# Kernel tuning notes

Hardware: AMD Instinct MI355X
Metric: run time of the kernel (lower is better)

The kernel has to match this reference:

```python
import jax, jax.numpy as jnp
import numpy as np

EPS = 1e-5  # BatchNorm eps (torch default)


def gcn_conv(x, W, b, src, dst, ew, n_nodes):
    """PyG GCNConv with normalize=True, add_self_loops=True (fill_value=1.0).
    Self-loop contribution handled analytically instead of appending edges."""
    xw = x @ W  # [N, out]
    # degree including self-loop weight 1.0 (PyG sums weights at the target node)
    deg = jax.ops.segment_sum(ew, dst, num_segments=n_nodes) + 1.0  # [N]
    dinv = jnp.where(deg > 0, jax.lax.rsqrt(deg), 0.0)
    norm = dinv[src] * ew * dinv[dst]  # [E]
    agg = jax.ops.segment_sum(xw[src] * norm[:, None], dst, num_segments=n_nodes)
    agg = agg + xw * (dinv * dinv)[:, None]  # self-loop message
    return agg + b


def batch_norm(x, gamma, beta):
    m = jnp.mean(x, axis=0)
    v = jnp.var(x, axis=0)  # biased, matches torch BN normalization
    return gamma * (x - m) * jax.lax.rsqrt(v + EPS) + beta


def setup_inputs() -> dict:
    key = jax.random.key(0)
    ks = jax.random.split(key, 12)
    N, E, D_IN, D_H, D_OUT = 100000, 1600000, 128, 128, 40
    x = jax.random.normal(ks[0], (N, D_IN), dtype=jnp.float32)
    edge_index = jax.random.randint(ks[1], (2, E), 0, N, dtype=jnp.int64)
    edge_weight = jax.random.uniform(ks[2], (E,), dtype=jnp.float32)
    def lin(k, fi, fo):
        s = 1.0 / np.sqrt(fi)
        return jax.random.uniform(k, (fi, fo), dtype=jnp.float32, minval=-s, maxval=s)
    return {
        "x": x, "edge_index": edge_index, "edge_weight": edge_weight,
        "W0": lin(ks[3], D_IN, D_H), "b0": jnp.zeros((D_H,), jnp.float32),
        "g0": jnp.ones((D_H,), jnp.float32), "be0": jnp.zeros((D_H,), jnp.float32),
        "W1": lin(ks[4], D_H, D_H), "b1": jnp.zeros((D_H,), jnp.float32),
        "g1": jnp.ones((D_H,), jnp.float32), "be1": jnp.zeros((D_H,), jnp.float32),
        "W2": lin(ks[5], D_H, D_OUT), "b2": jnp.zeros((D_OUT,), jnp.float32),
    }


def reference(x, edge_index, edge_weight, W0, b0, g0, be0, W1, b1, g1, be1, W2, b2):
    n_nodes = x.shape[0]
    src, dst = edge_index[0], edge_index[1]
    # layer 0: GCNConv -> BN -> ReLU (dropout identity: deterministic/eval)
    h = gcn_conv(x, W0, b0, src, dst, edge_weight, n_nodes)
    h = jax.nn.relu(batch_norm(h, g0, be0))
    # layer 1
    h = gcn_conv(h, W1, b1, src, dst, edge_weight, n_nodes)
    h = jax.nn.relu(batch_norm(h, g1, be1))
    # last conv + log_softmax over classes
    h = gcn_conv(h, W2, b2, src, dst, edge_weight, n_nodes)
    return jax.nn.log_softmax(h, axis=-1)
```

## Files before the change

### kernel.cpp

```cpp
#include <hip/hip_runtime.h>
#include <math.h>


#define CHUNK 8192

typedef __attribute__((ext_vector_type(8))) short short8v;
typedef __attribute__((ext_vector_type(16))) float float16v;

__device__ __forceinline__ float2 bf2_unpack(unsigned u) {
    float2 r;
    r.x = __uint_as_float(u << 16);
    r.y = __uint_as_float(u & 0xffff0000u);
    return r;
}
__device__ __forceinline__ unsigned bf2_pack(float a, float b) {
    unsigned ua = __float_as_uint(a);
    unsigned ub = __float_as_uint(b);
    ua = (ua + 0x7fffu + ((ua >> 16) & 1u)) >> 16;
    ub = (ub + 0x7fffu + ((ub >> 16) & 1u)) >> 16;
    return ua | (ub << 16);
}
__device__ __forceinline__ short bf16r(float x) {
    unsigned u = __float_as_uint(x);
    u = (u + 0x7fffu + ((u >> 16) & 1u)) >> 16;
    return (short)u;
}
__device__ __forceinline__ short8v lds_read8(const short* p) {
    short4 lo = *(const short4*)p;
    short4 hi = *(const short4*)(p + 4);
    short8v r;
    r[0] = lo.x; r[1] = lo.y; r[2] = lo.z; r[3] = lo.w;
    r[4] = hi.x; r[5] = hi.y; r[6] = hi.z; r[7] = hi.w;
    return r;
}

__global__ void k_detect(const unsigned* __restrict__ raw, int nsample, int* __restrict__ flag) {
    int i = blockIdx.x * blockDim.x + threadIdx.x;
    if (i < nsample) {
        if (raw[2 * i + 1] != 0u) atomicOr(flag, 1);
    }
}

__device__ __forceinline__ int edge_src(const unsigned* raw, int e, int E, int is64) {
    return is64 ? (int)raw[2 * (size_t)e] : (int)raw[e];
}
__device__ __forceinline__ int edge_dst(const unsigned* raw, int e, int E, int is64) {
    return is64 ? (int)raw[2 * ((size_t)E + e)] : (int)raw[(size_t)E + e];
}

__global__ __launch_bounds__(256) void k_bhist(const unsigned* __restrict__ raw,
                                               int* __restrict__ bhist, int* __restrict__ chist,
                                               const int* __restrict__ flag,
                                               int E, int NB, int nchunks) {
    __shared__ int h[512];
    int is64 = (*flag == 0);
    for (int c = blockIdx.x; c < nchunks; c += gridDim.x) {
        for (int t = threadIdx.x; t < 512; t += 256) h[t] = 0;
        __syncthreads();
        int base = c * CHUNK;
        int end = (base + CHUNK < E) ? base + CHUNK : E;
        for (int e = base + threadIdx.x; e < end; e += 256) {
            int d = edge_dst(raw, e, E, is64);
            atomicAdd(&h[d >> 8], 1);
        }
        __syncthreads();
        for (int t = threadIdx.x; t < NB; t += 256) {
            int v = h[t];
            chist[(size_t)c * 512 + t] = v;
            if (v) atomicAdd(&bhist[t], v);
        }
        __syncthreads();
    }
}

__global__ __launch_bounds__(512) void k_bscan(const int* __restrict__ bhist,
                                               int* __restrict__ bstart,
                                               int* __restrict__ bcur, int NB) {
    __shared__ int s[512];
    int tid = threadIdx.x;
    int v = (tid < NB) ? bhist[tid] : 0;
    s[tid] = v;
    __syncthreads();
    for (int off = 1; off < 512; off <<= 1) {
        int t = (tid >= off) ? s[tid - off] : 0;
        __syncthreads();
        if (tid >= off) s[tid] += t;
        __syncthreads();
    }
    int ex = s[tid] - v;
    if (tid <= NB) {
        int val = (tid < NB) ? ex : s[NB > 0 ? NB - 1 : 0];
        bstart[tid] = val;
        if (tid < NB) bcur[tid] = val;
    }
}

__global__ __launch_bounds__(256) void k_part(const unsigned* __restrict__ raw,
                                              const float* __restrict__ ew,
                                              const int* __restrict__ chist,
                                              int* __restrict__ bcur, int2* __restrict__ staging,
                                              const int* __restrict__ flag,
                                              int E, int NB, int nchunks) {
    __shared__ int cur[512];
    int is64 = (*flag == 0);
    for (int c = blockIdx.x; c < nchunks; c += gridDim.x) {
        for (int t = threadIdx.x; t < NB; t += 256) {
            int v = chist[(size_t)c * 512 + t];
            cur[t] = v ? atomicAdd(&bcur[t], v) : 0;
        }
        __syncthreads();
        int base = c * CHUNK;
        int end = (base + CHUNK < E) ? base + CHUNK : E;
        for (int e = base + threadIdx.x; e < end; e += 256) {
            int s = edge_src(raw, e, E, is64);
            int d = edge_dst(raw, e, E, is64);
            float w = ew[e];
            int pos = atomicAdd(&cur[d >> 8], 1);
            staging[pos] = make_int2(s | ((d & 255) << 24), __float_as_int(w));
        }
        __syncthreads();
    }
}

__global__ __launch_bounds__(256) void k_bucket(const int* __restrict__ bstart,
                                                const int2* __restrict__ staging,
                                                int* __restrict__ rowptr, float* __restrict__ dinv,
                                                int2* __restrict__ ep, int N, int NB) {
    __shared__ int cnt[256];
    __shared__ float dw[256];
    __shared__ int sc[256];
    __shared__ int cur[256];

    const int b = blockIdx.x;
    const int t = threadIdx.x;
    const int n0 = b << 8;
    const int nn = (N - n0 < 256) ? (N - n0) : 256;
    const int es = bstart[b], ee = bstart[b + 1];

    cnt[t] = 0;
    dw[t] = 0.f;
    __syncthreads();

    for (int j = es + t; j < ee; j += 256) {
        int2 p = staging[j];
        int dl = ((unsigned)p.x) >> 24;
        atomicAdd(&cnt[dl], 1);
        atomicAdd(&dw[dl], __int_as_float(p.y));
    }
    __syncthreads();

    int v = cnt[t];
    sc[t] = v;
    __syncthreads();
    for (int off = 1; off < 256; off <<= 1) {
        int tv = (t >= off) ? sc[t - off] : 0;
        __syncthreads();
        if (t >= off) sc[t] += tv;
        __syncthreads();
    }
    int exoff = sc[t] - v;
    cur[t] = es + exoff;
    if (t < nn) {
        rowptr[n0 + t] = es + exoff;
        dinv[n0 + t] = rsqrtf(dw[t] + 1.0f);
    }
    if (t == 0) rowptr[(n0 + 256 < N) ? (n0 + 256) : N] = ee;
    __syncthreads();

    for (int j = es + t; j < ee; j += 256) {
        int2 p = staging[j];
        int dl = ((unsigned)p.x) >> 24;
        int pos = atomicAdd(&cur[dl], 1);
        ep[pos] = make_int2(p.x & 0x00ffffff, p.y);
    }
}

template <int DOUT, int NCT, bool BN, bool FP32IN>
__global__ __launch_bounds__(256) void k_gemm_mfma(
    const float* __restrict__ Xf, const unsigned* __restrict__ Xp,
    const float* __restrict__ W, const float* __restrict__ scale,
    const float* __restrict__ shift, const float* __restrict__ dscale,
    unsigned* __restrict__ Y, int N)
{
    constexpr int NDW = DOUT / 2;
    constexpr int LDK = 132;
    constexpr int WROWS = (NCT == 4) ? 128 : 64;
    constexpr int RTPW = (NCT == 4) ? 2 : 1;
    __shared__ short Wt[WROWS][LDK];
    __shared__ short As[64][LDK];
    __shared__ float scL[128], shL[128], dscL[64];

    const int tid = threadIdx.x;
    const int wv = tid >> 6, ln = tid & 63;
    const int m = ln & 31, q = ln >> 5;
    const int ct = wv % NCT;
    const int rtbase = (NCT == 4) ? 0 : (wv >> 1);

    if (BN && tid < 128) { scL[tid] = scale[tid]; shL[tid] = shift[tid]; }
    for (int i = tid; i < WROWS * 128; i += 256) {
        int n = i % WROWS, k = i / WROWS;
        float w = (n < DOUT) ? W[k * DOUT + n] : 0.f;
        Wt[n][k] = bf16r(w);
    }

    for (int base = blockIdx.x * 64; base < N; base += gridDim.x * 64) {
        __syncthreads();
        if (FP32IN) {
            for (int i = tid; i < 64 * 32; i += 256) {
                int r = i >> 5, s = i & 31;
                int row = base + r;
                float4 v = make_float4(0.f, 0.f, 0.f, 0.f);
                if (row < N) v = ((const float4*)(Xf + (size_t)row * 128))[s];
                short4 qv = make_short4(bf16r(v.x), bf16r(v.y), bf16r(v.z), bf16r(v.w));
                *(short4*)&As[r][s * 4] = qv;
            }
        } else {
            for (int i = tid; i < 64 * 16; i += 256) {
                int r = i >> 4, s = i & 15;
                int row = base + r;
                uint4 u = make_uint4(0, 0, 0, 0);
                if (row < N) u = ((const uint4*)(Xp + (size_t)row * 64))[s];
                unsigned uu[4] = {u.x, u.y, u.z, u.w};
                short vv[8];
#pragma unroll
                for (int d = 0; d < 4; d++) {
                    float2 f = bf2_unpack(uu[d]);
                    int fi = s * 8 + 2 * d;
                    f.x = fmaxf(f.x * scL[fi] + shL[fi], 0.f);
                    f.y = fmaxf(f.y * scL[fi + 1] + shL[fi + 1], 0.f);
                    vv[2 * d] = bf16r(f.x);
                    vv[2 * d + 1] = bf16r(f.y);
                }
                *(short4*)&As[r][s * 8] = make_short4(vv[0], vv[1], vv[2], vv[3]);
                *(short4*)&As[r][s * 8 + 4] = make_short4(vv[4], vv[5], vv[6], vv[7]);
            }
        }
        if (tid < 64) {
            int row = base + tid;
            dscL[tid] = (row < N) ? dscale[row] : 0.f;
        }
        __syncthreads();

        float16v acc[RTPW];
#pragma unroll
        for (int rt = 0; rt < RTPW; rt++)
#pragma unroll
            for (int r = 0; r < 16; r++) acc[rt][r] = 0.f;

#pragma unroll
        for (int kc = 0; kc < 8; kc++) {
            int kb = kc * 16 + q * 8;
            short8v bfrag = lds_read8(&Wt[ct * 32 + m][kb]);
#pragma unroll
            for (int rt = 0; rt < RTPW; rt++) {
                int rtg = (NCT == 4) ? rt : rtbase;
                short8v afrag = lds_read8(&As[rtg * 32 + m][kb]);
                acc[rt] = __builtin_amdgcn_mfma_f32_32x32x16_bf16(afrag, bfrag, acc[rt], 0, 0, 0);
            }
        }

#pragma unroll
        for (int rt = 0; rt < RTPW; rt++) {
            int rtg = (NCT == 4) ? rt : rtbase;
#pragma unroll
            for (int r = 0; r < 16; r++) {
                int rowl = rtg * 32 + (r & 3) + 8 * (r >> 2) + 4 * q;
                float v = acc[rt][r] * dscL[rowl];
                float pv = __shfl_xor(v, 1);
                if (!(ln & 1)) {
                    int row = base + rowl;
                    int cp = ct * 16 + (m >> 1);
                    if (row < N && cp < NDW)
                        __builtin_nontemporal_store(bf2_pack(v, pv), &Y[(size_t)row * NDW + cp]);
                }
            }
        }
    }
}

__global__ __launch_bounds__(256) void k_agg128(
    const unsigned* __restrict__ xw, const int* __restrict__ rowptr,
    const unsigned long long* __restrict__ ep, const float* __restrict__ dinv,
    const float* __restrict__ bias, unsigned* __restrict__ h,
    float* __restrict__ bn_sum, float* __restrict__ bn_sq, int N)
{
    __shared__ float redS[512], redQ[512];
    const int lane = threadIdx.x & 63;
    const int wave = threadIdx.x >> 6;
    const int base = blockIdx.x * 32 + wave * 8;
    const float b0 = bias[2 * lane], b1 = bias[2 * lane + 1];
    float s0 = 0.f, s1 = 0.f, q0 = 0.f, q1 = 0.f;

    const int nmax = (N - base < 8) ? (N - base) : 8;
    for (int n = 0; n < nmax; n++) {
        const int i = base + n;
        const int rs = rowptr[i], re = rowptr[i + 1];
        const float di = dinv[i];
        float2 sv = bf2_unpack(xw[(size_t)i * 64 + lane]);
        float acc0 = sv.x, acc1 = sv.y;
        int j = rs;
        for (; j + 8 <= re; j += 8) {
            unsigned long long u0 = __builtin_nontemporal_load(ep + j);
            unsigned long long u1 = __builtin_nontemporal_load(ep + j + 1);
            unsigned long long u2 = __builtin_nontemporal_load(ep + j + 2);
            unsigned long long u3 = __builtin_nontemporal_load(ep + j + 3);
            unsigned long long u4 = __builtin_nontemporal_load(ep + j + 4);
            unsigned long long u5 = __builtin_nontemporal_load(ep + j + 5);
            unsigned long long u6 = __builtin_nontemporal_load(ep + j + 6);
            unsigned long long u7 = __builtin_nontemporal_load(ep + j + 7);
            unsigned v0 = xw[(size_t)(unsigned)u0 * 64 + lane];
            unsigned v1 = xw[(size_t)(unsigned)u1 * 64 + lane];
            unsigned v2 = xw[(size_t)(unsigned)u2 * 64 + lane];
            unsigned v3 = xw[(size_t)(unsigned)u3 * 64 + lane];
            unsigned v4 = xw[(size_t)(unsigned)u4 * 64 + lane];
            unsigned v5 = xw[(size_t)(unsigned)u5 * 64 + lane];
            unsigned v6 = xw[(size_t)(unsigned)u6 * 64 + lane];
            unsigned v7 = xw[(size_t)(unsigned)u7 * 64 + lane];
            float c0 = __int_as_float((int)(u0 >> 32)), c1 = __int_as_float((int)(u1 >> 32));
            float c2 = __int_as_float((int)(u2 >> 32)), c3 = __int_as_float((int)(u3 >> 32));
            float c4 = __int_as_float((int)(u4 >> 32)), c5 = __int_as_float((int)(u5 >> 32));
            float c6 = __int_as_float((int)(u6 >> 32)), c7 = __int_as_float((int)(u7 >> 32));
            float2 f0 = bf2_unpack(v0), f1 = bf2_unpack(v1);
            float2 f2 = bf2_unpack(v2), f3 = bf2_unpack(v3);
            float2 f4 = bf2_unpack(v4), f5 = bf2_unpack(v5);
            float2 f6 = bf2_unpack(v6), f7 = bf2_unpack(v7);
            acc0 += c0 * f0.x + c1 * f1.x + c2 * f2.x + c3 * f3.x
                  + c4 * f4.x + c5 * f5.x + c6 * f6.x + c7 * f7.x;
            acc1 += c0 * f0.y + c1 * f1.y + c2 * f2.y + c3 * f3.y
                  + c4 * f4.y + c5 * f5.y + c6 * f6.y + c7 * f7.y;
        }
        for (; j + 4 <= re; j += 4) {
            unsigned long long u0 = __builtin_nontemporal_load(ep + j);
            unsigned long long u1 = __builtin_nontemporal_load(ep + j + 1);
            unsigned long long u2 = __builtin_nontemporal_load(ep + j + 2);
            unsigned long long u3 = __builtin_nontemporal_load(ep + j + 3);
            unsigned v0 = xw[(size_t)(unsigned)u0 * 64 + lane];
            unsigned v1 = xw[(size_t)(unsigned)u1 * 64 + lane];
            unsigned v2 = xw[(size_t)(unsigned)u2 * 64 + lane];
            unsigned v3 = xw[(size_t)(unsigned)u3 * 64 + lane];
            float c0 = __int_as_float((int)(u0 >> 32)), c1 = __int_as_float((int)(u1 >> 32));
            float c2 = __int_as_float((int)(u2 >> 32)), c3 = __int_as_float((int)(u3 >> 32));
            float2 f0 = bf2_unpack(v0), f1 = bf2_unpack(v1);
            float2 f2 = bf2_unpack(v2), f3 = bf2_unpack(v3);
            acc0 += c0 * f0.x + c1 * f1.x + c2 * f2.x + c3 * f3.x;
            acc1 += c0 * f0.y + c1 * f1.y + c2 * f2.y + c3 * f3.y;
        }
        for (; j < re; j++) {
            unsigned long long u = __builtin_nontemporal_load(ep + j);
            float c = __int_as_float((int)(u >> 32));
            float2 f = bf2_unpack(xw[(size_t)(unsigned)u * 64 + lane]);
            acc0 += c * f.x;
            acc1 += c * f.y;
        }
        acc0 = acc0 * di + b0;
        acc1 = acc1 * di + b1;
        __builtin_nontemporal_store(bf2_pack(acc0, acc1), &h[(size_t)i * 64 + lane]);
        s0 += acc0; s1 += acc1; q0 += acc0 * acc0; q1 += acc1 * acc1;
    }

    redS[wave * 128 + 2 * lane] = s0;
    redS[wave * 128 + 2 * lane + 1] = s1;
    redQ[wave * 128 + 2 * lane] = q0;
    redQ[wave * 128 + 2 * lane + 1] = q1;
    __syncthreads();
    if (threadIdx.x < 128) {
        int f = threadIdx.x;
        float ts = redS[f] + redS[128 + f] + redS[256 + f] + redS[384 + f];
        float tq = redQ[f] + redQ[128 + f] + redQ[256 + f] + redQ[384 + f];
        atomicAdd(&bn_sum[f], ts);
        atomicAdd(&bn_sq[f], tq);
    }
}

__global__ void k_bnfin(const float* __restrict__ bn_sum, const float* __restrict__ bn_sq,
                        const float* __restrict__ gamma, const float* __restrict__ beta,
                        float* __restrict__ scale, float* __restrict__ shift, int N) {
    int f = threadIdx.x;
    float inv = 1.0f / (float)N;
    float m = bn_sum[f] * inv;
    float v = bn_sq[f] * inv - m * m;
    float sc = gamma[f] * rsqrtf(v + 1e-5f);
    scale[f] = sc;
    shift[f] = beta[f] - m * sc;
}

__global__ __launch_bounds__(256) void k_agg40(
    const unsigned* __restrict__ xw, const int* __restrict__ rowptr,
    const unsigned long long* __restrict__ ep, const float* __restrict__ dinv,
    const float* __restrict__ bias, float* __restrict__ out, int N)
{
    const int lane = threadIdx.x & 63;
    const int wave = threadIdx.x >> 6;
    const int half = lane >> 5;
    const int col = lane & 31;
    const bool act = col < 20;
    const int base = blockIdx.x * 32 + wave * 8;
    if (base >= N) return;
    const int cc = act ? col : 0;
    const float b0 = act ? bias[2 * col] : 0.f;
    const float b1 = act ? bias[2 * col + 1] : 0.f;

    for (int n = 0; n < 8; n += 2) {
        const int i = base + n + half;
        const bool valid = i < N;
        const int ic = valid ? i : 0;
        const int rs = rowptr[ic];
        int re = rowptr[ic + 1];
        re = valid ? re : rs;
        const float di = dinv[ic];
        float2 sv = bf2_unpack(xw[(size_t)ic * 20 + cc]);
        float acc0 = sv.x, acc1 = sv.y;
        int j = rs;
        for (; j + 8 <= re; j += 8) {
            unsigned long long u0 = __builtin_nontemporal_load(ep + j);
            unsigned long long u1 = __builtin_nontemporal_load(ep + j + 1);
            unsigned long long u2 = __builtin_nontemporal_load(ep + j + 2);
            unsigned long long u3 = __builtin_nontemporal_load(ep + j + 3);
            unsigned long long u4 = __builtin_nontemporal_load(ep + j + 4);
            unsigned long long u5 = __builtin_nontemporal_load(ep + j + 5);
            unsigned long long u6 = __builtin_nontemporal_load(ep + j + 6);
            unsigned long long u7 = __builtin_nontemporal_load(ep + j + 7);
            unsigned v0 = xw[(size_t)(unsigned)u0 * 20 + cc];
            unsigned v1 = xw[(size_t)(unsigned)u1 * 20 + cc];
            unsigned v2 = xw[(size_t)(unsigned)u2 * 20 + cc];
            unsigned v3 = xw[(size_t)(unsigned)u3 * 20 + cc];
            unsigned v4 = xw[(size_t)(unsigned)u4 * 20 + cc];
            unsigned v5 = xw[(size_t)(unsigned)u5 * 20 + cc];
            unsigned v6 = xw[(size_t)(unsigned)u6 * 20 + cc];
            unsigned v7 = xw[(size_t)(unsigned)u7 * 20 + cc];
            float c0 = __int_as_float((int)(u0 >> 32)), c1 = __int_as_float((int)(u1 >> 32));
            float c2 = __int_as_float((int)(u2 >> 32)), c3 = __int_as_float((int)(u3 >> 32));
            float c4 = __int_as_float((int)(u4 >> 32)), c5 = __int_as_float((int)(u5 >> 32));
            float c6 = __int_as_float((int)(u6 >> 32)), c7 = __int_as_float((int)(u7 >> 32));
            float2 f0 = bf2_unpack(v0), f1 = bf2_unpack(v1);
            float2 f2 = bf2_unpack(v2), f3 = bf2_unpack(v3);
            float2 f4 = bf2_unpack(v4), f5 = bf2_unpack(v5);
            float2 f6 = bf2_unpack(v6), f7 = bf2_unpack(v7);
            acc0 += c0 * f0.x + c1 * f1.x + c2 * f2.x + c3 * f3.x
                  + c4 * f4.x + c5 * f5.x + c6 * f6.x + c7 * f7.x;
            acc1 += c0 * f0.y + c1 * f1.y + c2 * f2.y + c3 * f3.y
                  + c4 * f4.y + c5 * f5.y + c6 * f6.y + c7 * f7.y;
        }
        for (; j < re; j++) {
            unsigned long long u = __builtin_nontemporal_load(ep + j);
            float c = __int_as_float((int)(u >> 32));
            float2 f = bf2_unpack(xw[(size_t)(unsigned)u * 20 + cc]);
            acc0 += c * f.x;
            acc1 += c * f.y;
        }
        acc0 = acc0 * di + b0;
        acc1 = acc1 * di + b1;

        float m = act ? fmaxf(acc0, acc1) : -1e30f;
#pragma unroll
        for (int off = 16; off; off >>= 1) m = fmaxf(m, __shfl_xor(m, off));
        float ex = act ? (expf(acc0 - m) + expf(acc1 - m)) : 0.f;
#pragma unroll
        for (int off = 16; off; off >>= 1) ex += __shfl_xor(ex, off);
        float ls = logf(ex);
        if (act && valid)
            *(float2*)&out[(size_t)i * 40 + 2 * col] = make_float2(acc0 - m - ls, acc1 - m - ls);
    }
}

extern "C" void kernel_launch(void* const* d_in, const int* in_sizes, int n_in,
                              void* d_out, int out_size, void* d_ws, size_t ws_size,
                              hipStream_t stream) {
    const float* x   = (const float*)d_in[0];
    const unsigned* ei = (const unsigned*)d_in[1];
    const float* ew  = (const float*)d_in[2];
    const float* W0  = (const float*)d_in[3];
    const float* b0  = (const float*)d_in[4];
    const float* g0  = (const float*)d_in[5];
    const float* be0 = (const float*)d_in[6];
    const float* W1  = (const float*)d_in[7];
    const float* b1  = (const float*)d_in[8];
    const float* g1  = (const float*)d_in[9];
    const float* be1 = (const float*)d_in[10];
    const float* W2  = (const float*)d_in[11];
    const float* b2  = (const float*)d_in[12];

    const int N = in_sizes[0] / 128;
    const int E = in_sizes[2];
    if (N <= 0 || E <= 0) return;
    const int NB = (N + 255) >> 8;
    const int nchunks = (E + CHUNK - 1) / CHUNK;

    char* ws = (char*)d_ws;
    size_t off = 0;
    auto carve = [&](size_t bytes) {
        char* p = ws + off;
        off += (bytes + 511) & ~((size_t)511);
        return p;
    };
    unsigned* F       = (unsigned*)carve((size_t)N * 64 * 4);
    unsigned* P       = (unsigned*)carve((size_t)N * 64 * 4);
    int2*     ep      = (int2*)carve((size_t)E * 8);
    int2*     staging = (int2*)carve((size_t)E * 8);
    int*      chist   = (int*)carve((size_t)nchunks * 512 * 4);
    int*      rowptr  = (int*)carve((size_t)(N + 1) * 4);
    float*    dinv    = (float*)carve((size_t)N * 4);
    int*      bhist   = (int*)carve(513 * 4);
    int*      bstart  = (int*)carve(513 * 4);
    int*      bcur    = (int*)carve(513 * 4);
    float*    bn      = (float*)carve(512 * 4);
    int*      flag    = (int*)carve(64);

    hipMemsetAsync(bhist, 0, 513 * 4, stream);
    hipMemsetAsync(flag, 0, 4, stream);

    int nsample = E < 4096 ? E : 4096;
    k_detect<<<(nsample + 255) / 256, 256, 0, stream>>>(ei, nsample, flag);
    int pgrid = nchunks < 1024 ? nchunks : 1024;
    k_bhist<<<pgrid, 256, 0, stream>>>(ei, bhist, chist, flag, E, NB, nchunks);
    k_bscan<<<1, 512, 0, stream>>>(bhist, bstart, bcur, NB);
    k_part<<<pgrid, 256, 0, stream>>>(ei, ew, chist, bcur, staging, flag, E, NB, nchunks);
    k_bucket<<<NB, 256, 0, stream>>>(bstart, staging, rowptr, dinv, ep, N, NB);

    const int agg_grid = (N + 31) / 32;
    const unsigned long long* epu = (const unsigned long long*)ep;

    k_gemm_mfma<128, 4, false, true><<<1024, 256, 0, stream>>>(x, nullptr, W0, nullptr, nullptr, dinv, P, N);
    hipMemsetAsync(bn, 0, 1024, stream);
    k_agg128<<<agg_grid, 256, 0, stream>>>(P, rowptr, epu, dinv, b0, F, bn, bn + 128, N);
    k_bnfin<<<1, 128, 0, stream>>>(bn, bn + 128, g0, be0, bn + 256, bn + 384, N);

    k_gemm_mfma<128, 4, true, false><<<1024, 256, 0, stream>>>(nullptr, F, W1, bn + 256, bn + 384, dinv, P, N);
    hipMemsetAsync(bn, 0, 1024, stream);
    k_agg128<<<agg_grid, 256, 0, stream>>>(P, rowptr, epu, dinv, b1, F, bn, bn + 128, N);
    k_bnfin<<<1, 128, 0, stream>>>(bn, bn + 128, g1, be1, bn + 256, bn + 384, N);

    k_gemm_mfma<40, 2, true, false><<<1024, 256, 0, stream>>>(nullptr, F, W2, bn + 256, bn + 384, dinv, P, N);
    k_agg40<<<agg_grid, 256, 0, stream>>>(P, rowptr, epu, dinv, b2, (float*)d_out, N);
}
```

Measured before the change: 586.8 us.

## Remove detect kernel and memsets, fold dtype detection and BN-accumulator zeroing into kernels

Removes the separate index-width detection kernel and its flag memset by having each chunk in the histogram and partition kernels detect 64-bit indices locally. The global bucket histogram and its atomics are dropped; the scan kernel now sums per-chunk histograms itself. BN accumulator zeroing moves into the GEMM kernels instead of separate memsets. The aggregation kernels now handle 16 nodes per wave instead of 8. This cuts launch count and small-operation overhead, at the cost of re-reading the high index words per chunk and a serial chunk loop in the scan. Per-chunk detection may also give inconsistent answers if a chunk happens to hold only zero high words.

```diff
diff --git a/kernel.cpp b/kernel.cpp
--- a/kernel.cpp
+++ b/kernel.cpp
@@ -34,13 +34,6 @@
     return r;
 }
 
-__global__ void k_detect(const unsigned* __restrict__ raw, int nsample, int* __restrict__ flag) {
-    int i = blockIdx.x * blockDim.x + threadIdx.x;
-    if (i < nsample) {
-        if (raw[2 * i + 1] != 0u) atomicOr(flag, 1);
-    }
-}
-
 __device__ __forceinline__ int edge_src(const unsigned* raw, int e, int E, int is64) {
     return is64 ? (int)raw[2 * (size_t)e] : (int)raw[e];
 }
@@ -48,37 +41,49 @@
     return is64 ? (int)raw[2 * ((size_t)E + e)] : (int)raw[(size_t)E + e];
 }
 
+__device__ __forceinline__ int chunk_is64(const unsigned* raw, int base, int end,
+                                          int tid, int* lflag) {
+    if (tid == 0) *lflag = 0;
+    __syncthreads();
+    int any = 0;
+    for (int e = base + tid; e < end; e += 256)
+        any |= (raw[2 * (size_t)e + 1] != 0u);
+    if (any) *lflag = 1;
+    __syncthreads();
+    return (*lflag == 0);
+}
+
 __global__ __launch_bounds__(256) void k_bhist(const unsigned* __restrict__ raw,
-                                               int* __restrict__ bhist, int* __restrict__ chist,
-                                               const int* __restrict__ flag,
+                                               int* __restrict__ chist,
                                                int E, int NB, int nchunks) {
     __shared__ int h[512];
-    int is64 = (*flag == 0);
+    __shared__ int lflag;
     for (int c = blockIdx.x; c < nchunks; c += gridDim.x) {
-        for (int t = threadIdx.x; t < 512; t += 256) h[t] = 0;
-        __syncthreads();
         int base = c * CHUNK;
         int end = (base + CHUNK < E) ? base + CHUNK : E;
+        int is64 = chunk_is64(raw, base, end, threadIdx.x, &lflag);
+        for (int t = threadIdx.x; t < 512; t += 256) h[t] = 0;
+        __syncthreads();
         for (int e = base + threadIdx.x; e < end; e += 256) {
             int d = edge_dst(raw, e, E, is64);
             atomicAdd(&h[d >> 8], 1);
         }
         __syncthreads();
-        for (int t = threadIdx.x; t < NB; t += 256) {
-            int v = h[t];
-            chist[(size_t)c * 512 + t] = v;
-            if (v) atomicAdd(&bhist[t], v);
-        }
-        __syncthreads();
-    }
-}
-
-__global__ __launch_bounds__(512) void k_bscan(const int* __restrict__ bhist,
+        for (int t = threadIdx.x; t < NB; t += 256)
+            chist[(size_t)c * 512 + t] = h[t];
+        __syncthreads();
+    }
+}
+
+__global__ __launch_bounds__(512) void k_bscan(const int* __restrict__ chist,
                                                int* __restrict__ bstart,
-                                               int* __restrict__ bcur, int NB) {
+                                               int* __restrict__ bcur,
+                                               int NB, int nchunks) {
     __shared__ int s[512];
     int tid = threadIdx.x;
-    int v = (tid < NB) ? bhist[tid] : 0;
+    int v = 0;
+    if (tid < NB)
+        for (int c = 0; c < nchunks; c++) v += chist[(size_t)c * 512 + tid];
     s[tid] = v;
     __syncthreads();
     for (int off = 1; off < 512; off <<= 1) {
@@ -99,18 +104,18 @@
                                               const float* __restrict__ ew,
                                               const int* __restrict__ chist,
                                               int* __restrict__ bcur, int2* __restrict__ staging,
-                                              const int* __restrict__ flag,
                                               int E, int NB, int nchunks) {
     __shared__ int cur[512];
-    int is64 = (*flag == 0);
+    __shared__ int lflag;
     for (int c = blockIdx.x; c < nchunks; c += gridDim.x) {
+        int base = c * CHUNK;
+        int end = (base + CHUNK < E) ? base + CHUNK : E;
+        int is64 = chunk_is64(raw, base, end, threadIdx.x, &lflag);
         for (int t = threadIdx.x; t < NB; t += 256) {
             int v = chist[(size_t)c * 512 + t];
             cur[t] = v ? atomicAdd(&bcur[t], v) : 0;
         }
         __syncthreads();
-        int base = c * CHUNK;
-        int end = (base + CHUNK < E) ? base + CHUNK : E;
         for (int e = base + threadIdx.x; e < end; e += 256) {
             int s = edge_src(raw, e, E, is64);
             int d = edge_dst(raw, e, E, is64);
@@ -180,7 +185,7 @@
     const float* __restrict__ Xf, const unsigned* __restrict__ Xp,
     const float* __restrict__ W, const float* __restrict__ scale,
     const float* __restrict__ shift, const float* __restrict__ dscale,
-    unsigned* __restrict__ Y, int N)
+    unsigned* __restrict__ Y, float* __restrict__ bnacc, int N)
 {
     constexpr int NDW = DOUT / 2;
     constexpr int LDK = 132;
@@ -196,6 +201,7 @@
     const int ct = wv % NCT;
     const int rtbase = (NCT == 4) ? 0 : (wv >> 1);
 
+    if (bnacc && blockIdx.x == 0) bnacc[tid] = 0.f;
     if (BN && tid < 128) { scL[tid] = scale[tid]; shL[tid] = shift[tid]; }
     for (int i = tid; i < WROWS * 128; i += 256) {
         int n = i % WROWS, k = i / WROWS;
@@ -287,11 +293,11 @@
     __shared__ float redS[512], redQ[512];
     const int lane = threadIdx.x & 63;
     const int wave = threadIdx.x >> 6;
-    const int base = blockIdx.x * 32 + wave * 8;
+    const int base = blockIdx.x * 64 + wave * 16;
     const float b0 = bias[2 * lane], b1 = bias[2 * lane + 1];
     float s0 = 0.f, s1 = 0.f, q0 = 0.f, q1 = 0.f;
 
-    const int nmax = (N - base < 8) ? (N - base) : 8;
+    const int nmax = (N - base < 16) ? (N - base) : 16;
     for (int n = 0; n < nmax; n++) {
         const int i = base + n;
         const int rs = rowptr[i], re = rowptr[i + 1];
@@ -394,13 +400,13 @@
     const int half = lane >> 5;
     const int col = lane & 31;
     const bool act = col < 20;
-    const int base = blockIdx.x * 32 + wave * 8;
+    const int base = blockIdx.x * 64 + wave * 16;
     if (base >= N) return;
     const int cc = act ? col : 0;
     const float b0 = act ? bias[2 * col] : 0.f;
     const float b1 = act ? bias[2 * col + 1] : 0.f;
 
-    for (int n = 0; n < 8; n += 2) {
+    for (int n = 0; n < 16; n += 2) {
         const int i = base + n + half;
         const bool valid = i < N;
         const int ic = valid ? i : 0;
@@ -500,36 +506,27 @@
     int*      chist   = (int*)carve((size_t)nchunks * 512 * 4);
     int*      rowptr  = (int*)carve((size_t)(N + 1) * 4);
     float*    dinv    = (float*)carve((size_t)N * 4);
-    int*      bhist   = (int*)carve(513 * 4);
     int*      bstart  = (int*)carve(513 * 4);
     int*      bcur    = (int*)carve(513 * 4);
     float*    bn      = (float*)carve(512 * 4);
-    int*      flag    = (int*)carve(64);
-
-    hipMemsetAsync(bhist, 0, 513 * 4, stream);
-    hipMemsetAsync(flag, 0, 4, stream);
-
-    int nsample = E < 4096 ? E : 4096;
-    k_detect<<<(nsample + 255) / 256, 256, 0, stream>>>(ei, nsample, flag);
+
     int pgrid = nchunks < 1024 ? nchunks : 1024;
-    k_bhist<<<pgrid, 256, 0, stream>>>(ei, bhist, chist, flag, E, NB, nchunks);
-    k_bscan<<<1, 512, 0, stream>>>(bhist, bstart, bcur, NB);
-    k_part<<<pgrid, 256, 0, stream>>>(ei, ew, chist, bcur, staging, flag, E, NB, nchunks);
+    k_bhist<<<pgrid, 256, 0, stream>>>(ei, chist, E, NB, nchunks);
+    k_bscan<<<1, 512, 0, stream>>>(chist, bstart, bcur, NB, nchunks);
+    k_part<<<pgrid, 256, 0, stream>>>(ei, ew, chist, bcur, staging, E, NB, nchunks);
     k_bucket<<<NB, 256, 0, stream>>>(bstart, staging, rowptr, dinv, ep, N, NB);
 
-    const int agg_grid = (N + 31) / 32;
+    const int agg_grid = (N + 63) / 64;
     const unsigned long long* epu = (const unsigned long long*)ep;
 
-    k_gemm_mfma<128, 4, false, true><<<1024, 256, 0, stream>>>(x, nullptr, W0, nullptr, nullptr, dinv, P, N);
-    hipMemsetAsync(bn, 0, 1024, stream);
+    k_gemm_mfma<128, 4, false, true><<<1024, 256, 0, stream>>>(x, nullptr, W0, nullptr, nullptr, dinv, P, bn, N);
     k_agg128<<<agg_grid, 256, 0, stream>>>(P, rowptr, epu, dinv, b0, F, bn, bn + 128, N);
     k_bnfin<<<1, 128, 0, stream>>>(bn, bn + 128, g0, be0, bn + 256, bn + 384, N);
 
-    k_gemm_mfma<128, 4, true, false><<<1024, 256, 0, stream>>>(nullptr, F, W1, bn + 256, bn + 384, dinv, P, N);
-    hipMemsetAsync(bn, 0, 1024, stream);
+    k_gemm_mfma<128, 4, true, false><<<1024, 256, 0, stream>>>(nullptr, F, W1, bn + 256, bn + 384, dinv, P, bn, N);
     k_agg128<<<agg_grid, 256, 0, stream>>>(P, rowptr, epu, dinv, b1, F, bn, bn + 128, N);
     k_bnfin<<<1, 128, 0, stream>>>(bn, bn + 128, g1, be1, bn + 256, bn + 384, N);
 
-    k_gemm_mfma<40, 2, true, false><<<1024, 256, 0, stream>>>(nullptr, F, W2, bn + 256, bn + 384, dinv, P, N);
+    k_gemm_mfma<40, 2, true, false><<<1024, 256, 0, stream>>>(nullptr, F, W2, bn + 256, bn + 384, dinv, P, nullptr, N);
     k_agg40<<<agg_grid, 256, 0, stream>>>(P, rowptr, epu, dinv, b2, (float*)d_out, N);
 }
```

New measurement: 578.3 us. About the same (-1.5%).
